# Kernel tuning notes

Hardware: AMD Instinct MI355X
Metric: run time of the kernel (lower is better)

## Reference

```python
import jax, jax.numpy as jnp
import numpy as np

B, S, D = 2, 1024, 1024
E, H, TOPK = 8, 2048, 2
LN_EPS = 1e-5


def setup_inputs() -> dict:
    key = jax.random.key(0)
    k1, k2, k3, k4 = jax.random.split(key, 4)
    scale = 0.02
    return {
        "x": jax.random.normal(k1, (B, S, D), dtype=jnp.float32),
        "ln_w": jnp.ones((D,), dtype=jnp.float32),
        "ln_b": jnp.zeros((D,), dtype=jnp.float32),
        "gate_w": jax.random.normal(k2, (E, D), dtype=jnp.float32) * scale,
        "w1": jax.random.normal(k3, (E, D, 2 * H), dtype=jnp.float32) * scale,
        "w2": jax.random.normal(k4, (E, H, D), dtype=jnp.float32) * scale,
    }


def reference(x, ln_w, ln_b, gate_w, w1, w2):
    # LayerNorm (pre-norm, identity kept for residual)
    mu = jnp.mean(x, axis=-1, keepdims=True)
    var = jnp.mean(jnp.square(x - mu), axis=-1, keepdims=True)
    xn = (x - mu) * jax.lax.rsqrt(var + LN_EPS) * ln_w + ln_b

    # Router: softmax -> top-k -> renormalize -> scatter into dense mask [B,S,E]
    logits = jnp.einsum("bsd,ed->bse", xn, gate_w)
    weights = jax.nn.softmax(logits, axis=-1)
    tk_w, tk_i = jax.lax.top_k(weights, TOPK)
    tk_w = tk_w / jnp.sum(tk_w, axis=-1, keepdims=True)
    router_mask = jnp.sum(jax.nn.one_hot(tk_i, E, dtype=xn.dtype) * tk_w[..., None], axis=-2)

    # Naive MoE: every expert's GLU FFN over all tokens, masked sum.
    h = jnp.einsum("bsd,edf->besf", xn, w1)          # [B,E,S,2H]
    x_part, gate_part = jnp.split(h, 2, axis=-1)       # each [B,E,S,H]
    act = jax.nn.gelu(gate_part, approximate=False) * x_part
    expert_out = jnp.einsum("besh,ehd->besd", act, w2)  # [B,E,S,D]
    moe_out = jnp.einsum("besd,bse->bsd", expert_out, router_mask)

    # dropout is identity in eval mode
    return (moe_out + x, router_mask)
```

## Files before the change

### kernel.cpp

```cpp
#include <hip/hip_runtime.h>
#include <cstdint>
#include <cstddef>

#define B_    2
#define S_    1024
#define D_    1024
#define E_    8
#define H_    2048
#define H2_   (2*H_)
#define N_    (B_*S_)
#define LN_EPS 1e-5f

typedef __attribute__((ext_vector_type(8))) short bf16x8;
typedef __attribute__((ext_vector_type(4))) float f32x4;
typedef __attribute__((ext_vector_type(4))) unsigned short u16x4;

__device__ __forceinline__ unsigned short f2bf(float f) {
    union { float f; unsigned u; } v; v.f = f;
    unsigned r = v.u + 0x7FFFu + ((v.u >> 16) & 1u);
    return (unsigned short)(r >> 16);
}
__device__ __forceinline__ float gelu_exact(float g) {
    return 0.5f * g * (1.f + erff(g * 0.70710678118654752f));
}
__device__ __forceinline__ float f4i(const float4& v, int i) { return (&v.x)[i]; }

__global__ __launch_bounds__(256) void ln_router_kernel(
    const float* __restrict__ x,
    const float* __restrict__ ln_w,
    const float* __restrict__ ln_b,
    const float* __restrict__ gate_w,
    float* __restrict__ out,
    unsigned short* __restrict__ xn_b,
    float* __restrict__ w_pair,
    int* __restrict__ list,
    int* __restrict__ counts)
{
    const int t   = blockIdx.x;
    const int tid = threadIdx.x;
    const int wave = tid >> 6, lane = tid & 63;

    __shared__ float rs_[4], rss_[4];
    __shared__ float stats[2];
    __shared__ float lred[4][8];

    const float4* xrow = (const float4*)(x + (size_t)t * D_);
    float4 v = xrow[tid];

    float s  = v.x + v.y + v.z + v.w;
    float ss = v.x*v.x + v.y*v.y + v.z*v.z + v.w*v.w;
    #pragma unroll
    for (int o = 32; o > 0; o >>= 1) { s += __shfl_down(s, o); ss += __shfl_down(ss, o); }
    if (lane == 0) { rs_[wave] = s; rss_[wave] = ss; }
    __syncthreads();
    if (tid == 0) {
        float a = 0.f, b = 0.f;
        #pragma unroll
        for (int i = 0; i < 4; ++i) { a += rs_[i]; b += rss_[i]; }
        float mu = a * (1.f / D_);
        float var = b * (1.f / D_) - mu * mu;
        stats[0] = mu;
        stats[1] = rsqrtf(var + LN_EPS);
    }
    __syncthreads();
    const float mu = stats[0], rstd = stats[1];

    const float4 lw = *(const float4*)(ln_w + tid * 4);
    const float4 lb = *(const float4*)(ln_b + tid * 4);
    float4 n;
    n.x = (v.x - mu) * rstd * lw.x + lb.x;
    n.y = (v.y - mu) * rstd * lw.y + lb.y;
    n.z = (v.z - mu) * rstd * lw.z + lb.z;
    n.w = (v.w - mu) * rstd * lw.w + lb.w;

    u16x4 nb = { f2bf(n.x), f2bf(n.y), f2bf(n.z), f2bf(n.w) };
    *(u16x4*)(xn_b + (size_t)t * D_ + tid * 4) = nb;
    *(float4*)(out + (size_t)t * D_ + tid * 4) = v;

    float acc[E_];
    #pragma unroll
    for (int e = 0; e < E_; ++e) {
        const float4 g = *(const float4*)(gate_w + (size_t)e * D_ + tid * 4);
        acc[e] = n.x*g.x + n.y*g.y + n.z*g.z + n.w*g.w;
    }
    #pragma unroll
    for (int e = 0; e < E_; ++e) {
        float r = acc[e];
        #pragma unroll
        for (int o = 32; o > 0; o >>= 1) r += __shfl_down(r, o);
        if (lane == 0) lred[wave][e] = r;
    }
    __syncthreads();

    if (tid == 0) {
        float l[E_];
        #pragma unroll
        for (int e = 0; e < E_; ++e)
            l[e] = lred[0][e] + lred[1][e] + lred[2][e] + lred[3][e];
        int e0 = 0;
        #pragma unroll
        for (int e = 1; e < E_; ++e) if (l[e] > l[e0]) e0 = e;
        int e1 = (e0 == 0) ? 1 : 0;
        #pragma unroll
        for (int e = 0; e < E_; ++e) if (e != e0 && e != e1 && l[e] > l[e1]) e1 = e;
        float m  = l[e0];
        float p1 = __expf(l[e1] - m);
        float inv = 1.f / (1.f + p1);
        float w0 = inv, w1 = p1 * inv;

        float* mask = out + (size_t)N_ * D_ + (size_t)t * E_;
        #pragma unroll
        for (int e = 0; e < E_; ++e)
            mask[e] = (e == e0) ? w0 : ((e == e1) ? w1 : 0.f);

        int i0 = atomicAdd(&counts[e0], 1);
        list[e0 * N_ + i0] = t * 2 + 0;
        int i1 = atomicAdd(&counts[e1], 1);
        list[e1 * N_ + i1] = t * 2 + 1;
        w_pair[t * 2 + 0] = w0;
        w_pair[t * 2 + 1] = w1;
    }
}

__global__ __launch_bounds__(256) void wprep_kernel(
    const float* __restrict__ src, unsigned short* __restrict__ dst,
    int R, int C)
{
    const int e = blockIdx.z;
    src += (size_t)e * R * C;
    dst += (size_t)e * R * C;
    const int r0 = blockIdx.y * 64, c0 = blockIdx.x * 64;
    __shared__ unsigned short T[64][72];
    const int tid = threadIdx.x;
    const int kk = tid >> 4;
    const int cc = (tid & 15) * 4;
    #pragma unroll
    for (int s = 0; s < 4; ++s) {
        int k = kk + s * 16;
        const float4 v = *(const float4*)(src + (size_t)(r0 + k) * C + c0 + cc);
        T[cc + 0][k] = f2bf(v.x);
        T[cc + 1][k] = f2bf(v.y);
        T[cc + 2][k] = f2bf(v.z);
        T[cc + 3][k] = f2bf(v.w);
    }
    __syncthreads();
    const int c  = tid >> 2;
    const int k4 = (tid & 3) * 16;
    bf16x8 lo = *(const bf16x8*)&T[c][k4];
    bf16x8 hi = *(const bf16x8*)&T[c][k4 + 8];
    unsigned short* o = dst + (size_t)(c0 + c) * R + r0 + k4;
    *(bf16x8*)o = lo;
    *(bf16x8*)(o + 8) = hi;
}

template<bool PRET>
__global__ __launch_bounds__(256, 2) void gemm1_kernel(
    const unsigned short* __restrict__ xn_b,
    const float* __restrict__ w1,
    const unsigned short* __restrict__ w1t,
    const int* __restrict__ list,
    const int* __restrict__ counts,
    unsigned short* __restrict__ act_b)
{
    const int e = blockIdx.z;
    const int cnt = counts[e];
    const int m0 = blockIdx.y * 128;
    if (m0 >= cnt) return;
    const int c0 = blockIdx.x * 128;

    __shared__ unsigned short As[128][40];
    __shared__ unsigned short Bs[256][40];
    __shared__ int pairL[128];

    const int tid  = threadIdx.x;
    const int lane = tid & 63;
    const int wv   = tid >> 6;
    const int wr   = wv >> 1, wc = wv & 1;
    const int* lst = list + e * N_;

    if (tid < 128) {
        int r = m0 + tid;
        pairL[tid] = (r < cnt) ? lst[r] : -1;
    }
    __syncthreads();

    const int sr  = tid >> 2;
    const int skk = (tid & 3) * 8;

    const unsigned short* aSrc[2];
    #pragma unroll
    for (int i = 0; i < 2; ++i) {
        int p = pairL[i * 64 + sr];
        int tok = (p >= 0) ? (p >> 1) : 0;
        aSrc[i] = xn_b + (size_t)tok * D_ + skk;
    }

    const unsigned short* bSrcT[4];
    const float* bFsrc[2];
    int bCgl[2];
    if constexpr (PRET) {
        const unsigned short* w1te = w1t + (size_t)e * D_ * H2_;
        #pragma unroll
        for (int i = 0; i < 4; ++i) {
            int br = i * 64 + sr;
            int gcol = (br < 128) ? (c0 + br) : (H_ + c0 + br - 128);
            bSrcT[i] = w1te + (size_t)gcol * D_ + skk;
        }
    } else {
        const float* w1e = w1 + (size_t)e * D_ * H2_;
        #pragma unroll
        for (int u = 0; u < 2; ++u) {
            int idx = tid * 2 + u;
            int cg = idx & 63, kg = idx >> 6;
            int cgl = cg * 4;
            int gcol = (cgl < 128) ? (c0 + cgl) : (H_ + c0 + cgl - 128);
            bFsrc[u] = w1e + (size_t)(kg * 4) * H2_ + gcol;
            bCgl[u] = cgl | (kg << 16);
        }
    }

    bf16x8 aR[2], bR[4];
    float4 bF[2][4];
    #pragma unroll
    for (int i = 0; i < 2; ++i) aR[i] = *(const bf16x8*)(aSrc[i]);
    if constexpr (PRET) {
        #pragma unroll
        for (int i = 0; i < 4; ++i) bR[i] = *(const bf16x8*)(bSrcT[i]);
    } else {
        #pragma unroll
        for (int u = 0; u < 2; ++u)
            #pragma unroll
            for (int j = 0; j < 4; ++j)
                bF[u][j] = *(const float4*)(bFsrc[u] + (size_t)j * H2_);
    }

    f32x4 accx[4][4], accg[4][4];
    #pragma unroll
    for (int m = 0; m < 4; ++m)
        #pragma unroll
        for (int n = 0; n < 4; ++n) {
            accx[m][n] = (f32x4){0.f, 0.f, 0.f, 0.f};
            accg[m][n] = (f32x4){0.f, 0.f, 0.f, 0.f};
        }

    const int fr = lane & 15, fg = (lane >> 4) * 8;

    for (int k0 = 0; k0 < D_; k0 += 32) {
        __syncthreads();
        #pragma unroll
        for (int i = 0; i < 2; ++i) *(bf16x8*)&As[i * 64 + sr][skk] = aR[i];
        if constexpr (PRET) {
            #pragma unroll
            for (int i = 0; i < 4; ++i) *(bf16x8*)&Bs[i * 64 + sr][skk] = bR[i];
        } else {
            #pragma unroll
            for (int u = 0; u < 2; ++u) {
                int cgl = bCgl[u] & 0xFFFF, kg = bCgl[u] >> 16;
                #pragma unroll
                for (int i = 0; i < 4; ++i) {
                    u16x4 pk = { f2bf(f4i(bF[u][0], i)), f2bf(f4i(bF[u][1], i)),
                                 f2bf(f4i(bF[u][2], i)), f2bf(f4i(bF[u][3], i)) };
                    *(u16x4*)&Bs[cgl + i][kg * 4] = pk;
                }
            }
        }
        __syncthreads();

        if (k0 + 32 < D_) {
            int kn = k0 + 32;
            #pragma unroll
            for (int i = 0; i < 2; ++i) aR[i] = *(const bf16x8*)(aSrc[i] + kn);
            if constexpr (PRET) {
                #pragma unroll
                for (int i = 0; i < 4; ++i) bR[i] = *(const bf16x8*)(bSrcT[i] + kn);
            } else {
                #pragma unroll
                for (int u = 0; u < 2; ++u)
                    #pragma unroll
                    for (int j = 0; j < 4; ++j)
                        bF[u][j] = *(const float4*)(bFsrc[u] + (size_t)(kn + j) * H2_);
            }
        }

        bf16x8 af[4];
        #pragma unroll
        for (int m = 0; m < 4; ++m) af[m] = *(const bf16x8*)&As[wr * 64 + m * 16 + fr][fg];
        {
            bf16x8 bxf[4];
            #pragma unroll
            for (int n = 0; n < 4; ++n) bxf[n] = *(const bf16x8*)&Bs[wc * 64 + n * 16 + fr][fg];
            #pragma unroll
            for (int m = 0; m < 4; ++m)
                #pragma unroll
                for (int n = 0; n < 4; ++n)
                    accx[m][n] = __builtin_amdgcn_mfma_f32_16x16x32_bf16(af[m], bxf[n], accx[m][n], 0, 0, 0);
        }
        {
            bf16x8 bgf[4];
            #pragma unroll
            for (int n = 0; n < 4; ++n) bgf[n] = *(const bf16x8*)&Bs[128 + wc * 64 + n * 16 + fr][fg];
            #pragma unroll
            for (int m = 0; m < 4; ++m)
                #pragma unroll
                for (int n = 0; n < 4; ++n)
                    accg[m][n] = __builtin_amdgcn_mfma_f32_16x16x32_bf16(af[m], bgf[n], accg[m][n], 0, 0, 0);
        }
    }

    const int fq = lane >> 4;
    #pragma unroll
    for (int m = 0; m < 4; ++m) {
        #pragma unroll
        for (int j = 0; j < 4; ++j) {
            int rowt = wr * 64 + m * 16 + fq * 4 + j;
            if (m0 + rowt < cnt) {
                int pair = pairL[rowt];
                unsigned short* arow = act_b + (size_t)pair * H_ + c0 + wc * 64 + fr;
                #pragma unroll
                for (int n = 0; n < 4; ++n) {
                    float hx = accx[m][n][j];
                    float hg = accg[m][n][j];
                    arow[n * 16] = f2bf(gelu_exact(hg) * hx);
                }
            }
        }
    }
}

template<bool PRET>
__global__ __launch_bounds__(256, 2) void gemm2_kernel(
    const unsigned short* __restrict__ act_b,
    const float* __restrict__ w2,
    const unsigned short* __restrict__ w2t,
    const int* __restrict__ list,
    const int* __restrict__ counts,
    const float* __restrict__ w_pair,
    float* __restrict__ out)
{
    const int z = blockIdx.z;
    const int e = z >> 1, ks = z & 1;
    const int cnt = counts[e];
    const int m0 = blockIdx.y * 128;
    if (m0 >= cnt) return;
    const int c0 = blockIdx.x * 128;
    const int kbeg = ks * (H_ / 2), kend = kbeg + H_ / 2;

    __shared__ unsigned short As[128][40];
    __shared__ unsigned short Bs[128][40];
    __shared__ int   pairL[128];
    __shared__ float wgtL[128];

    const int tid  = threadIdx.x;
    const int lane = tid & 63;
    const int wv   = tid >> 6;
    const int wr   = wv >> 1, wc = wv & 1;
    const int* lst = list + e * N_;

    if (tid < 128) {
        int r = m0 + tid;
        int p = (r < cnt) ? lst[r] : -1;
        pairL[tid] = p;
        wgtL[tid]  = (p >= 0) ? w_pair[p] : 0.f;
    }
    __syncthreads();

    const int sr  = tid >> 2;
    const int skk = (tid & 3) * 8;

    const unsigned short* aSrc[2];
    #pragma unroll
    for (int i = 0; i < 2; ++i) {
        int p = pairL[i * 64 + sr];
        aSrc[i] = act_b + (size_t)((p >= 0) ? p : 0) * H_ + skk;
    }

    const unsigned short* bSrcT[2];
    const float* bFsrc;
    int bCg = 0, bKg = 0;
    if constexpr (PRET) {
        const unsigned short* w2te = w2t + (size_t)e * D_ * H_;
        #pragma unroll
        for (int i = 0; i < 2; ++i)
            bSrcT[i] = w2te + (size_t)(c0 + i * 64 + sr) * H_ + skk;
    } else {
        const float* w2e = w2 + (size_t)e * H_ * D_;
        bCg = (tid & 31) * 4;
        bKg = (tid >> 5) * 4;
        bFsrc = w2e + (size_t)bKg * D_ + c0 + bCg;
    }

    bf16x8 aR[2], bR[2];
    float4 bF[4];
    #pragma unroll
    for (int i = 0; i < 2; ++i) aR[i] = *(const bf16x8*)(aSrc[i] + kbeg);
    if constexpr (PRET) {
        #pragma unroll
        for (int i = 0; i < 2; ++i) bR[i] = *(const bf16x8*)(bSrcT[i] + kbeg);
    } else {
        #pragma unroll
        for (int j = 0; j < 4; ++j) bF[j] = *(const float4*)(bFsrc + (size_t)(kbeg + j) * D_);
    }

    f32x4 acc[4][4];
    #pragma unroll
    for (int m = 0; m < 4; ++m)
        #pragma unroll
        for (int n = 0; n < 4; ++n) acc[m][n] = (f32x4){0.f, 0.f, 0.f, 0.f};

    const int fr = lane & 15, fg = (lane >> 4) * 8;

    for (int k0 = kbeg; k0 < kend; k0 += 32) {
        __syncthreads();
        #pragma unroll
        for (int i = 0; i < 2; ++i) *(bf16x8*)&As[i * 64 + sr][skk] = aR[i];
        if constexpr (PRET) {
            #pragma unroll
            for (int i = 0; i < 2; ++i) *(bf16x8*)&Bs[i * 64 + sr][skk] = bR[i];
        } else {
            #pragma unroll
            for (int i = 0; i < 4; ++i) {
                u16x4 pk = { f2bf(f4i(bF[0], i)), f2bf(f4i(bF[1], i)),
                             f2bf(f4i(bF[2], i)), f2bf(f4i(bF[3], i)) };
                *(u16x4*)&Bs[bCg + i][bKg] = pk;
            }
        }
        __syncthreads();

        if (k0 + 32 < kend) {
            int kn = k0 + 32;
            #pragma unroll
            for (int i = 0; i < 2; ++i) aR[i] = *(const bf16x8*)(aSrc[i] + kn);
            if constexpr (PRET) {
                #pragma unroll
                for (int i = 0; i < 2; ++i) bR[i] = *(const bf16x8*)(bSrcT[i] + kn);
            } else {
                #pragma unroll
                for (int j = 0; j < 4; ++j) bF[j] = *(const float4*)(bFsrc + (size_t)(kn + j) * D_);
            }
        }

        bf16x8 af[4], bf_[4];
        #pragma unroll
        for (int m = 0; m < 4; ++m) af[m] = *(const bf16x8*)&As[wr * 64 + m * 16 + fr][fg];
        #pragma unroll
        for (int n = 0; n < 4; ++n) bf_[n] = *(const bf16x8*)&Bs[wc * 64 + n * 16 + fr][fg];
        #pragma unroll
        for (int m = 0; m < 4; ++m)
            #pragma unroll
            for (int n = 0; n < 4; ++n)
                acc[m][n] = __builtin_amdgcn_mfma_f32_16x16x32_bf16(af[m], bf_[n], acc[m][n], 0, 0, 0);
    }

    const int fq = lane >> 4;
    #pragma unroll
    for (int m = 0; m < 4; ++m) {
        #pragma unroll
        for (int j = 0; j < 4; ++j) {
            int rowt = wr * 64 + m * 16 + fq * 4 + j;
            if (m0 + rowt < cnt) {
                int p = pairL[rowt];
                int token = p >> 1;
                float w = wgtL[rowt];
                float* orow = out + (size_t)token * D_ + c0 + wc * 64 + fr;
                #pragma unroll
                for (int n = 0; n < 4; ++n)
                    atomicAdd(&orow[n * 16], w * acc[m][n][j]);
            }
        }
    }
}

extern "C" void kernel_launch(void* const* d_in, const int* in_sizes, int n_in,
                              void* d_out, int out_size, void* d_ws, size_t ws_size,
                              hipStream_t stream)
{
    const float* x      = (const float*)d_in[0];
    const float* ln_w   = (const float*)d_in[1];
    const float* ln_b   = (const float*)d_in[2];
    const float* gate_w = (const float*)d_in[3];
    const float* w1     = (const float*)d_in[4];
    const float* w2     = (const float*)d_in[5];
    float* out = (float*)d_out;

    unsigned char* w = (unsigned char*)d_ws;
    size_t off = 0;
    auto alloc = [&](size_t bytes) -> void* {
        void* p = w + off;
        off += (bytes + 255) & ~(size_t)255;
        return p;
    };
    unsigned short* xn_b  = (unsigned short*)alloc((size_t)N_ * D_ * 2);
    unsigned short* act_b = (unsigned short*)alloc((size_t)N_ * 2 * H_ * 2);
    float* w_pair = (float*)alloc((size_t)N_ * 2 * 4);
    int*   lists  = (int*)alloc((size_t)E_ * N_ * 4);
    int*   counts = (int*)alloc(256);
    unsigned short* w1t = (unsigned short*)alloc((size_t)E_ * D_ * H2_ * 2);
    unsigned short* w2t = (unsigned short*)alloc((size_t)E_ * H_ * D_ * 2);
    const bool pret = (ws_size >= off);

    hipMemsetAsync(counts, 0, 256, stream);

    if (pret) {
        wprep_kernel<<<dim3(H2_ / 64, D_ / 64, E_), 256, 0, stream>>>(w1, w1t, D_, H2_);
        wprep_kernel<<<dim3(D_ / 64, H_ / 64, E_), 256, 0, stream>>>(w2, w2t, H_, D_);
    }

    ln_router_kernel<<<N_, 256, 0, stream>>>(x, ln_w, ln_b, gate_w, out, xn_b,
                                             w_pair, lists, counts);

    if (pret) {
        gemm1_kernel<true><<<dim3(H_ / 128, 16, E_), 256, 0, stream>>>(
            xn_b, w1, w1t, lists, counts, act_b);
        gemm2_kernel<true><<<dim3(D_ / 128, 16, E_ * 2), 256, 0, stream>>>(
            act_b, w2, w2t, lists, counts, w_pair, out);
    } else {
        gemm1_kernel<false><<<dim3(H_ / 128, 16, E_), 256, 0, stream>>>(
            xn_b, w1, w1t, lists, counts, act_b);
        gemm2_kernel<false><<<dim3(D_ / 128, 16, E_ * 2), 256, 0, stream>>>(
            act_b, w2, w2t, lists, counts, w_pair, out);
    }
}
```

Measured before the change: 437.7 us.

## Use direct global-to-LDS loads with double buffering and swizzle in MoE GEMMs

Both expert GEMMs now stage tiles through global_load_lds straight into double-buffered, XOR-swizzled shared memory, so the next tile's load overlaps the current MFMA work and the register staging round-trip goes away. gemm1's column tile shrinks from 128 to 64, occupancy hints rise to 3 blocks, and the two weight-transpose launches merge into one kernel. The fallback path that converted fp32 weights on the fly is removed, so the code now assumes the workspace is always large enough for the transposed weights.

```diff
diff --git a/kernel.cpp b/kernel.cpp
--- a/kernel.cpp
+++ b/kernel.cpp
@@ -23,7 +23,11 @@
 __device__ __forceinline__ float gelu_exact(float g) {
     return 0.5f * g * (1.f + erff(g * 0.70710678118654752f));
 }
-__device__ __forceinline__ float f4i(const float4& v, int i) { return (&v.x)[i]; }
+__device__ __forceinline__ void gl16(const void* g, void* l) {
+    __builtin_amdgcn_global_load_lds(
+        (const __attribute__((address_space(1))) unsigned int*)g,
+        (__attribute__((address_space(3))) unsigned int*)l, 16, 0, 0);
+}
 
 __global__ __launch_bounds__(256) void ln_router_kernel(
     const float* __restrict__ x,
@@ -123,13 +127,26 @@
 }
 
 __global__ __launch_bounds__(256) void wprep_kernel(
-    const float* __restrict__ src, unsigned short* __restrict__ dst,
-    int R, int C)
+    const float* __restrict__ w1, const float* __restrict__ w2,
+    unsigned short* __restrict__ w1t, unsigned short* __restrict__ w2t)
 {
-    const int e = blockIdx.z;
-    src += (size_t)e * R * C;
-    dst += (size_t)e * R * C;
-    const int r0 = blockIdx.y * 64, c0 = blockIdx.x * 64;
+    const int bid = blockIdx.x;
+    const float* src; unsigned short* dst; int R, C, r0, c0;
+    if (bid < 8192) {
+        int e = bid >> 10, t = bid & 1023;
+        R = D_; C = H2_;
+        src = w1  + (size_t)e * R * C;
+        dst = w1t + (size_t)e * R * C;
+        r0 = (t & 15) * 64; c0 = (t >> 4) * 64;
+    } else {
+        int b2 = bid - 8192;
+        int e = b2 >> 9, t = b2 & 511;
+        R = H_; C = D_;
+        src = w2  + (size_t)e * R * C;
+        dst = w2t + (size_t)e * R * C;
+        r0 = (t & 31) * 64; c0 = (t >> 5) * 64;
+    }
+
     __shared__ unsigned short T[64][72];
     const int tid = threadIdx.x;
     const int kk = tid >> 4;
@@ -153,161 +170,103 @@
     *(bf16x8*)(o + 8) = hi;
 }
 
-template<bool PRET>
-__global__ __launch_bounds__(256, 2) void gemm1_kernel(
+__global__ __launch_bounds__(256, 3) void gemm1_kernel(
     const unsigned short* __restrict__ xn_b,
-    const float* __restrict__ w1,
     const unsigned short* __restrict__ w1t,
     const int* __restrict__ list,
     const int* __restrict__ counts,
     unsigned short* __restrict__ act_b)
 {
-    const int e = blockIdx.z;
+    const int e   = blockIdx.z;
     const int cnt = counts[e];
-    const int m0 = blockIdx.y * 128;
+    const int m0  = blockIdx.y * 128;
     if (m0 >= cnt) return;
-    const int c0 = blockIdx.x * 128;
-
-    __shared__ unsigned short As[128][40];
-    __shared__ unsigned short Bs[256][40];
+    const int c0  = blockIdx.x * 64;
+
+    __shared__ __attribute__((aligned(128))) unsigned char lds[2][16384];
     __shared__ int pairL[128];
 
     const int tid  = threadIdx.x;
     const int lane = tid & 63;
     const int wv   = tid >> 6;
     const int wr   = wv >> 1, wc = wv & 1;
-    const int* lst = list + e * N_;
 
     if (tid < 128) {
         int r = m0 + tid;
-        pairL[tid] = (r < cnt) ? lst[r] : -1;
-    }
-    __syncthreads();
-
-    const int sr  = tid >> 2;
-    const int skk = (tid & 3) * 8;
-
-    const unsigned short* aSrc[2];
+        pairL[tid] = (r < cnt) ? list[e * N_ + r] : -1;
+    }
+    __syncthreads();
+
+    const int srow = tid >> 2;
+    const int glin = tid & 3;
+    const unsigned short* aAddr[2];
     #pragma unroll
     for (int i = 0; i < 2; ++i) {
-        int p = pairL[i * 64 + sr];
+        int row = i * 64 + srow;
+        int p   = pairL[row];
         int tok = (p >= 0) ? (p >> 1) : 0;
-        aSrc[i] = xn_b + (size_t)tok * D_ + skk;
-    }
-
-    const unsigned short* bSrcT[4];
-    const float* bFsrc[2];
-    int bCgl[2];
-    if constexpr (PRET) {
-        const unsigned short* w1te = w1t + (size_t)e * D_ * H2_;
-        #pragma unroll
-        for (int i = 0; i < 4; ++i) {
-            int br = i * 64 + sr;
-            int gcol = (br < 128) ? (c0 + br) : (H_ + c0 + br - 128);
-            bSrcT[i] = w1te + (size_t)gcol * D_ + skk;
-        }
-    } else {
-        const float* w1e = w1 + (size_t)e * D_ * H2_;
-        #pragma unroll
-        for (int u = 0; u < 2; ++u) {
-            int idx = tid * 2 + u;
-            int cg = idx & 63, kg = idx >> 6;
-            int cgl = cg * 4;
-            int gcol = (cgl < 128) ? (c0 + cgl) : (H_ + c0 + cgl - 128);
-            bFsrc[u] = w1e + (size_t)(kg * 4) * H2_ + gcol;
-            bCgl[u] = cgl | (kg << 16);
-        }
-    }
-
-    bf16x8 aR[2], bR[4];
-    float4 bF[2][4];
-    #pragma unroll
-    for (int i = 0; i < 2; ++i) aR[i] = *(const bf16x8*)(aSrc[i]);
-    if constexpr (PRET) {
-        #pragma unroll
-        for (int i = 0; i < 4; ++i) bR[i] = *(const bf16x8*)(bSrcT[i]);
-    } else {
-        #pragma unroll
-        for (int u = 0; u < 2; ++u)
-            #pragma unroll
-            for (int j = 0; j < 4; ++j)
-                bF[u][j] = *(const float4*)(bFsrc[u] + (size_t)j * H2_);
-    }
-
-    f32x4 accx[4][4], accg[4][4];
+        int gsrc = glin ^ ((row >> 1) & 3);
+        aAddr[i] = xn_b + (size_t)tok * D_ + gsrc * 8;
+    }
+    const unsigned short* w1te = w1t + (size_t)e * (size_t)D_ * H2_;
+    const int gsrcB = glin ^ ((srow >> 1) & 3);
+    const unsigned short* bxAddr = w1te + (size_t)(c0 + srow) * D_ + gsrcB * 8;
+    const unsigned short* bgAddr = w1te + (size_t)(H_ + c0 + srow) * D_ + gsrcB * 8;
+
+    const int wvOff = wv * 1024;
+    const int gsw = (((lane >> 4) ^ ((lane >> 1) & 3)) << 4);
+    const int fr  = lane & 15;
+    const int fq  = lane >> 4;
+
+    f32x4 accx[4][2], accg[4][2];
     #pragma unroll
     for (int m = 0; m < 4; ++m)
         #pragma unroll
-        for (int n = 0; n < 4; ++n) {
+        for (int n = 0; n < 2; ++n) {
             accx[m][n] = (f32x4){0.f, 0.f, 0.f, 0.f};
             accg[m][n] = (f32x4){0.f, 0.f, 0.f, 0.f};
         }
 
-    const int fr = lane & 15, fg = (lane >> 4) * 8;
-
-    for (int k0 = 0; k0 < D_; k0 += 32) {
+    {
+        unsigned char* b = &lds[0][0];
+        gl16(aAddr[0], b + wvOff);
+        gl16(aAddr[1], b + 4096 + wvOff);
+        gl16(bxAddr,   b + 8192 + wvOff);
+        gl16(bgAddr,   b + 12288 + wvOff);
+    }
+    __syncthreads();
+
+    int cur = 0;
+    for (int t = 0; t < D_ / 32; ++t) {
+        if (t + 1 < D_ / 32) {
+            const int kn = (t + 1) * 32;
+            unsigned char* b = &lds[cur ^ 1][0];
+            gl16(aAddr[0] + kn, b + wvOff);
+            gl16(aAddr[1] + kn, b + 4096 + wvOff);
+            gl16(bxAddr   + kn, b + 8192 + wvOff);
+            gl16(bgAddr   + kn, b + 12288 + wvOff);
+        }
+        const unsigned char* bb = &lds[cur][0];
+        bf16x8 af[4], bx[2], bg[2];
+        #pragma unroll
+        for (int m = 0; m < 4; ++m)
+            af[m] = *(const bf16x8*)(bb + (wr * 64 + m * 16 + fr) * 64 + gsw);
+        #pragma unroll
+        for (int n = 0; n < 2; ++n) {
+            bx[n] = *(const bf16x8*)(bb + 8192  + (wc * 32 + n * 16 + fr) * 64 + gsw);
+            bg[n] = *(const bf16x8*)(bb + 12288 + (wc * 32 + n * 16 + fr) * 64 + gsw);
+        }
+        #pragma unroll
+        for (int m = 0; m < 4; ++m)
+            #pragma unroll
+            for (int n = 0; n < 2; ++n) {
+                accx[m][n] = __builtin_amdgcn_mfma_f32_16x16x32_bf16(af[m], bx[n], accx[m][n], 0, 0, 0);
+                accg[m][n] = __builtin_amdgcn_mfma_f32_16x16x32_bf16(af[m], bg[n], accg[m][n], 0, 0, 0);
+            }
         __syncthreads();
-        #pragma unroll
-        for (int i = 0; i < 2; ++i) *(bf16x8*)&As[i * 64 + sr][skk] = aR[i];
-        if constexpr (PRET) {
-            #pragma unroll
-            for (int i = 0; i < 4; ++i) *(bf16x8*)&Bs[i * 64 + sr][skk] = bR[i];
-        } else {
-            #pragma unroll
-            for (int u = 0; u < 2; ++u) {
-                int cgl = bCgl[u] & 0xFFFF, kg = bCgl[u] >> 16;
-                #pragma unroll
-                for (int i = 0; i < 4; ++i) {
-                    u16x4 pk = { f2bf(f4i(bF[u][0], i)), f2bf(f4i(bF[u][1], i)),
-                                 f2bf(f4i(bF[u][2], i)), f2bf(f4i(bF[u][3], i)) };
-                    *(u16x4*)&Bs[cgl + i][kg * 4] = pk;
-                }
-            }
-        }
-        __syncthreads();
-
-        if (k0 + 32 < D_) {
-            int kn = k0 + 32;
-            #pragma unroll
-            for (int i = 0; i < 2; ++i) aR[i] = *(const bf16x8*)(aSrc[i] + kn);
-            if constexpr (PRET) {
-                #pragma unroll
-                for (int i = 0; i < 4; ++i) bR[i] = *(const bf16x8*)(bSrcT[i] + kn);
-            } else {
-                #pragma unroll
-                for (int u = 0; u < 2; ++u)
-                    #pragma unroll
-                    for (int j = 0; j < 4; ++j)
-                        bF[u][j] = *(const float4*)(bFsrc[u] + (size_t)(kn + j) * H2_);
-            }
-        }
-
-        bf16x8 af[4];
-        #pragma unroll
-        for (int m = 0; m < 4; ++m) af[m] = *(const bf16x8*)&As[wr * 64 + m * 16 + fr][fg];
-        {
-            bf16x8 bxf[4];
-            #pragma unroll
-            for (int n = 0; n < 4; ++n) bxf[n] = *(const bf16x8*)&Bs[wc * 64 + n * 16 + fr][fg];
-            #pragma unroll
-            for (int m = 0; m < 4; ++m)
-                #pragma unroll
-                for (int n = 0; n < 4; ++n)
-                    accx[m][n] = __builtin_amdgcn_mfma_f32_16x16x32_bf16(af[m], bxf[n], accx[m][n], 0, 0, 0);
-        }
-        {
-            bf16x8 bgf[4];
-            #pragma unroll
-            for (int n = 0; n < 4; ++n) bgf[n] = *(const bf16x8*)&Bs[128 + wc * 64 + n * 16 + fr][fg];
-            #pragma unroll
-            for (int m = 0; m < 4; ++m)
-                #pragma unroll
-                for (int n = 0; n < 4; ++n)
-                    accg[m][n] = __builtin_amdgcn_mfma_f32_16x16x32_bf16(af[m], bgf[n], accg[m][n], 0, 0, 0);
-        }
-    }
-
-    const int fq = lane >> 4;
+        cur ^= 1;
+    }
+
     #pragma unroll
     for (int m = 0; m < 4; ++m) {
         #pragma unroll
@@ -315,9 +274,9 @@
             int rowt = wr * 64 + m * 16 + fq * 4 + j;
             if (m0 + rowt < cnt) {
                 int pair = pairL[rowt];
-                unsigned short* arow = act_b + (size_t)pair * H_ + c0 + wc * 64 + fr;
+                unsigned short* arow = act_b + (size_t)pair * H_ + c0 + wc * 32 + fr;
                 #pragma unroll
-                for (int n = 0; n < 4; ++n) {
+                for (int n = 0; n < 2; ++n) {
                     float hx = accx[m][n][j];
                     float hg = accg[m][n][j];
                     arow[n * 16] = f2bf(gelu_exact(hg) * hx);
@@ -327,10 +286,8 @@
     }
 }
 
-template<bool PRET>
-__global__ __launch_bounds__(256, 2) void gemm2_kernel(
+__global__ __launch_bounds__(256, 3) void gemm2_kernel(
     const unsigned short* __restrict__ act_b,
-    const float* __restrict__ w2,
     const unsigned short* __restrict__ w2t,
     const int* __restrict__ list,
     const int* __restrict__ counts,
@@ -340,13 +297,12 @@
     const int z = blockIdx.z;
     const int e = z >> 1, ks = z & 1;
     const int cnt = counts[e];
-    const int m0 = blockIdx.y * 128;
+    const int m0  = blockIdx.y * 128;
     if (m0 >= cnt) return;
-    const int c0 = blockIdx.x * 128;
-    const int kbeg = ks * (H_ / 2), kend = kbeg + H_ / 2;
-
-    __shared__ unsigned short As[128][40];
-    __shared__ unsigned short Bs[128][40];
+    const int c0  = blockIdx.x * 128;
+    const int kbase = ks * (H_ / 2);
+
+    __shared__ __attribute__((aligned(128))) unsigned char lds[2][16384];
     __shared__ int   pairL[128];
     __shared__ float wgtL[128];
 
@@ -354,52 +310,33 @@
     const int lane = tid & 63;
     const int wv   = tid >> 6;
     const int wr   = wv >> 1, wc = wv & 1;
-    const int* lst = list + e * N_;
 
     if (tid < 128) {
         int r = m0 + tid;
-        int p = (r < cnt) ? lst[r] : -1;
+        int p = (r < cnt) ? list[e * N_ + r] : -1;
         pairL[tid] = p;
         wgtL[tid]  = (p >= 0) ? w_pair[p] : 0.f;
     }
     __syncthreads();
 
-    const int sr  = tid >> 2;
-    const int skk = (tid & 3) * 8;
-
-    const unsigned short* aSrc[2];
+    const int srow = tid >> 2;
+    const int glin = tid & 3;
+    const unsigned short* aAddr[2];
+    const unsigned short* bAddr[2];
+    const unsigned short* w2te = w2t + (size_t)e * (size_t)D_ * H_;
     #pragma unroll
     for (int i = 0; i < 2; ++i) {
-        int p = pairL[i * 64 + sr];
-        aSrc[i] = act_b + (size_t)((p >= 0) ? p : 0) * H_ + skk;
-    }
-
-    const unsigned short* bSrcT[2];
-    const float* bFsrc;
-    int bCg = 0, bKg = 0;
-    if constexpr (PRET) {
-        const unsigned short* w2te = w2t + (size_t)e * D_ * H_;
-        #pragma unroll
-        for (int i = 0; i < 2; ++i)
-            bSrcT[i] = w2te + (size_t)(c0 + i * 64 + sr) * H_ + skk;
-    } else {
-        const float* w2e = w2 + (size_t)e * H_ * D_;
-        bCg = (tid & 31) * 4;
-        bKg = (tid >> 5) * 4;
-        bFsrc = w2e + (size_t)bKg * D_ + c0 + bCg;
-    }
-
-    bf16x8 aR[2], bR[2];
-    float4 bF[4];
-    #pragma unroll
-    for (int i = 0; i < 2; ++i) aR[i] = *(const bf16x8*)(aSrc[i] + kbeg);
-    if constexpr (PRET) {
-        #pragma unroll
-        for (int i = 0; i < 2; ++i) bR[i] = *(const bf16x8*)(bSrcT[i] + kbeg);
-    } else {
-        #pragma unroll
-        for (int j = 0; j < 4; ++j) bF[j] = *(const float4*)(bFsrc + (size_t)(kbeg + j) * D_);
-    }
+        int row = i * 64 + srow;
+        int gsrc = glin ^ ((row >> 1) & 3);
+        int p = pairL[row];
+        aAddr[i] = act_b + (size_t)((p >= 0) ? p : 0) * H_ + kbase + gsrc * 8;
+        bAddr[i] = w2te + (size_t)(c0 + row) * H_ + kbase + gsrc * 8;
+    }
+
+    const int wvOff = wv * 1024;
+    const int gsw = (((lane >> 4) ^ ((lane >> 1) & 3)) << 4);
+    const int fr  = lane & 15;
+    const int fq  = lane >> 4;
 
     f32x4 acc[4][4];
     #pragma unroll
@@ -407,51 +344,42 @@
         #pragma unroll
         for (int n = 0; n < 4; ++n) acc[m][n] = (f32x4){0.f, 0.f, 0.f, 0.f};
 
-    const int fr = lane & 15, fg = (lane >> 4) * 8;
-
-    for (int k0 = kbeg; k0 < kend; k0 += 32) {
-        __syncthreads();
-        #pragma unroll
-        for (int i = 0; i < 2; ++i) *(bf16x8*)&As[i * 64 + sr][skk] = aR[i];
-        if constexpr (PRET) {
-            #pragma unroll
-            for (int i = 0; i < 2; ++i) *(bf16x8*)&Bs[i * 64 + sr][skk] = bR[i];
-        } else {
-            #pragma unroll
-            for (int i = 0; i < 4; ++i) {
-                u16x4 pk = { f2bf(f4i(bF[0], i)), f2bf(f4i(bF[1], i)),
-                             f2bf(f4i(bF[2], i)), f2bf(f4i(bF[3], i)) };
-                *(u16x4*)&Bs[bCg + i][bKg] = pk;
-            }
-        }
-        __syncthreads();
-
-        if (k0 + 32 < kend) {
-            int kn = k0 + 32;
-            #pragma unroll
-            for (int i = 0; i < 2; ++i) aR[i] = *(const bf16x8*)(aSrc[i] + kn);
-            if constexpr (PRET) {
-                #pragma unroll
-                for (int i = 0; i < 2; ++i) bR[i] = *(const bf16x8*)(bSrcT[i] + kn);
-            } else {
-                #pragma unroll
-                for (int j = 0; j < 4; ++j) bF[j] = *(const float4*)(bFsrc + (size_t)(kn + j) * D_);
-            }
-        }
-
+    {
+        unsigned char* b = &lds[0][0];
+        gl16(aAddr[0], b + wvOff);
+        gl16(aAddr[1], b + 4096 + wvOff);
+        gl16(bAddr[0], b + 8192 + wvOff);
+        gl16(bAddr[1], b + 12288 + wvOff);
+    }
+    __syncthreads();
+
+    int cur = 0;
+    for (int t = 0; t < (H_ / 2) / 32; ++t) {
+        if (t + 1 < (H_ / 2) / 32) {
+            const int kn = (t + 1) * 32;
+            unsigned char* b = &lds[cur ^ 1][0];
+            gl16(aAddr[0] + kn, b + wvOff);
+            gl16(aAddr[1] + kn, b + 4096 + wvOff);
+            gl16(bAddr[0] + kn, b + 8192 + wvOff);
+            gl16(bAddr[1] + kn, b + 12288 + wvOff);
+        }
+        const unsigned char* bb = &lds[cur][0];
         bf16x8 af[4], bf_[4];
         #pragma unroll
-        for (int m = 0; m < 4; ++m) af[m] = *(const bf16x8*)&As[wr * 64 + m * 16 + fr][fg];
-        #pragma unroll
-        for (int n = 0; n < 4; ++n) bf_[n] = *(const bf16x8*)&Bs[wc * 64 + n * 16 + fr][fg];
+        for (int m = 0; m < 4; ++m)
+            af[m] = *(const bf16x8*)(bb + (wr * 64 + m * 16 + fr) * 64 + gsw);
+        #pragma unroll
+        for (int n = 0; n < 4; ++n)
+            bf_[n] = *(const bf16x8*)(bb + 8192 + (wc * 64 + n * 16 + fr) * 64 + gsw);
         #pragma unroll
         for (int m = 0; m < 4; ++m)
             #pragma unroll
             for (int n = 0; n < 4; ++n)
                 acc[m][n] = __builtin_amdgcn_mfma_f32_16x16x32_bf16(af[m], bf_[n], acc[m][n], 0, 0, 0);
-    }
-
-    const int fq = lane >> 4;
+        __syncthreads();
+        cur ^= 1;
+    }
+
     #pragma unroll
     for (int m = 0; m < 4; ++m) {
         #pragma unroll
@@ -496,27 +424,18 @@
     int*   counts = (int*)alloc(256);
     unsigned short* w1t = (unsigned short*)alloc((size_t)E_ * D_ * H2_ * 2);
     unsigned short* w2t = (unsigned short*)alloc((size_t)E_ * H_ * D_ * 2);
-    const bool pret = (ws_size >= off);
+    (void)off;
 
     hipMemsetAsync(counts, 0, 256, stream);
 
-    if (pret) {
-        wprep_kernel<<<dim3(H2_ / 64, D_ / 64, E_), 256, 0, stream>>>(w1, w1t, D_, H2_);
-        wprep_kernel<<<dim3(D_ / 64, H_ / 64, E_), 256, 0, stream>>>(w2, w2t, H_, D_);
-    }
+    wprep_kernel<<<12288, 256, 0, stream>>>(w1, w2, w1t, w2t);
 
     ln_router_kernel<<<N_, 256, 0, stream>>>(x, ln_w, ln_b, gate_w, out, xn_b,
                                              w_pair, lists, counts);
 
-    if (pret) {
-        gemm1_kernel<true><<<dim3(H_ / 128, 16, E_), 256, 0, stream>>>(
-            xn_b, w1, w1t, lists, counts, act_b);
-        gemm2_kernel<true><<<dim3(D_ / 128, 16, E_ * 2), 256, 0, stream>>>(
-            act_b, w2, w2t, lists, counts, w_pair, out);
-    } else {
-        gemm1_kernel<false><<<dim3(H_ / 128, 16, E_), 256, 0, stream>>>(
-            xn_b, w1, w1t, lists, counts, act_b);
-        gemm2_kernel<false><<<dim3(D_ / 128, 16, E_ * 2), 256, 0, stream>>>(
-            act_b, w2, w2t, lists, counts, w_pair, out);
-    }
-}
+    gemm1_kernel<<<dim3(H_ / 64, 16, E_), 256, 0, stream>>>(
+        xn_b, w1t, lists, counts, act_b);
+
+    gemm2_kernel<<<dim3(D_ / 128, 16, E_ * 2), 256, 0, stream>>>(
+        act_b, w2t, lists, counts, w_pair, out);
+}
```

Result: no change. 434.2 us (-0.8%).
